# Kernel tuning notes

Hardware: AMD Instinct MI355X
Metric: run time of the kernel (lower is better)

Reference implementation:

```python
import jax, jax.numpy as jnp
import numpy as np

B, L, D, H, OUT = 4, 2048, 1024, 8, 256
DH = D // H
EPS = 1e-12


def setup_inputs() -> dict:
    key = jax.random.key(0)
    ks = jax.random.split(key, 20)
    s = lambda fan_in: 1.0 / np.sqrt(fan_in)
    def lin(k, fin, fout):
        k1, k2 = jax.random.split(k)
        w = jax.random.uniform(k1, (fin, fout), jnp.float32, -s(fin), s(fin))
        b = jax.random.uniform(k2, (fout,), jnp.float32, -s(fin), s(fin))
        return w, b
    x = jax.random.normal(ks[0], (B, L, D), jnp.float32)
    wq, bq = lin(ks[1], D, D)
    wk, bk = lin(ks[2], D, D)
    wv, bv = lin(ks[3], D, D)
    gamma = jnp.ones((D,), jnp.float32)
    beta = jnp.zeros((D,), jnp.float32)
    wff, bff = lin(ks[4], D, D)
    wc1, bc1 = lin(ks[5], D, D)
    wc2, bc2 = lin(ks[6], D, 1)
    wl1, bl1 = lin(ks[7], L, L)
    wl2, bl2 = lin(ks[8], L, OUT)
    return dict(x=x, wq=wq, bq=bq, wk=wk, bk=bk, wv=wv, bv=bv,
                gamma=gamma, beta=beta, wff=wff, bff=bff,
                wc1=wc1, bc1=bc1, wc2=wc2, bc2=bc2,
                wl1=wl1, bl1=bl1, wl2=wl2, bl2=bl2)


def layernorm(x, gamma, beta):
    mean = x.mean(-1, keepdims=True)
    var = ((x - mean) ** 2).mean(-1, keepdims=True)  # biased variance
    return gamma * (x - mean) / jnp.sqrt(var + EPS) + beta


def reference(x, wq, bq, wk, bk, wv, bv, gamma, beta, wff, bff,
              wc1, bc1, wc2, bc2, wl1, bl1, wl2, bl2):
    # multi-head self-attention (dropout = identity at inference)
    q = (x @ wq + bq).reshape(B, L, H, DH)
    k = (x @ wk + bk).reshape(B, L, H, DH)
    v = (x @ wv + bv).reshape(B, L, H, DH)
    scores = jnp.einsum('bqhd,bkhd->bhqk', q, k) / np.sqrt(DH)
    attn = jax.nn.softmax(scores, axis=-1)                  # [B,H,L,L]
    ctx = jnp.einsum('bhqk,bkhd->bqhd', attn, v).reshape(B, L, D)
    h = layernorm(x + ctx, gamma, beta)
    # feedforward: Linear + ReLU (hidden = d_model), residual + same layernorm params
    ff = jax.nn.relu(h @ wff + bff)
    h = layernorm(h + ff, gamma, beta)
    # collapse d_model -> 1
    c = jax.nn.relu(h @ wc1 + bc1)
    c = jax.nn.relu(c @ wc2 + bc2)                          # [B,L,1]
    c = jnp.squeeze(c, axis=-1)                             # [B,L]
    # collapse length -> out_featuresize
    c = jax.nn.relu(c @ wl1 + bl1)
    out = c @ wl2 + bl2                                     # [B,OUT]
    return out
```

## Files before the change

### kernel.cpp

```cpp
#include <hip/hip_runtime.h>

typedef unsigned short u16;
typedef unsigned int u32;
typedef __attribute__((ext_vector_type(4))) float f32x4;
typedef __attribute__((ext_vector_type(8))) short short8;
typedef __attribute__((ext_vector_type(4))) u32 u32x4;
typedef __attribute__((ext_vector_type(4))) u16 u16x4;

#define BB 4
#define LL 2048
#define DD 1024
#define HH 8
#define DHH 128

__device__ __forceinline__ u16 f2b(float f) {
  u32 u = __builtin_bit_cast(u32, f);
  u += 0x7fffu + ((u >> 16) & 1u);
  return (u16)(u >> 16);
}
__device__ __forceinline__ float b2f(u16 h) {
  u32 u = ((u32)h) << 16;
  return __builtin_bit_cast(float, u);
}
__device__ __forceinline__ float exp2_fast(float x) {
  float r;
  asm("v_exp_f32 %0, %1" : "=v"(r) : "v"(x));
  return r;
}
__device__ __forceinline__ u32 packbf(float a, float b) {
  return (u32)f2b(a) | ((u32)f2b(b) << 16);
}
__device__ __forceinline__ u32 bperm(int srcLane, u32 v) {
  return (u32)__builtin_amdgcn_ds_bpermute(srcLane << 2, (int)v);
}

#define GLDS16(g, l)                                                          \
  __builtin_amdgcn_global_load_lds(                                           \
      (const __attribute__((address_space(1))) void*)(g),                     \
      (__attribute__((address_space(3))) void*)(l), 16, 0, 0)

__global__ __launch_bounds__(256) void cvt_k(const float* __restrict__ X,
                                             u16* __restrict__ Xb, long n) {
  long i = ((long)blockIdx.x * 256 + threadIdx.x) * 4;
  if (i >= n) return;
  f32x4 v = *(const f32x4*)(X + i);
  u16x4 o;
#pragma unroll
  for (int k = 0; k < 4; k++) o[k] = f2b(v[k]);
  *(u16x4*)(Xb + i) = o;
}

__global__ __launch_bounds__(256) void tr_k(const float* __restrict__ W,
                                            u16* __restrict__ WT) {
  __shared__ float tile[32][33];
  const int bx = blockIdx.x, by = blockIdx.y;
  const int tx = threadIdx.x & 31, ty = threadIdx.x >> 5;
#pragma unroll
  for (int i = 0; i < 4; i++)
    tile[ty + i * 8][tx] =
        W[(long)(by * 32 + ty + i * 8) * 1024 + bx * 32 + tx];
  __syncthreads();
#pragma unroll
  for (int i = 0; i < 4; i++)
    WT[(long)(bx * 32 + ty + i * 8) * 1024 + by * 32 + tx] =
        f2b(tile[tx][ty + i * 8]);
}

template <bool RELU, int OMODE>
__global__ __launch_bounds__(256, 2) void gemm_k(
    const u16* __restrict__ A, const u16* __restrict__ BT,
    const float* __restrict__ bias, float scale, float* __restrict__ Cf,
    u16* __restrict__ Cb, int M, int N, int K) {
  __shared__ u16 As[128 * 32];
  __shared__ u16 Bs[128 * 32];
  const int nwg = gridDim.x * gridDim.y;
  const int bid = blockIdx.x + blockIdx.y * gridDim.x;
  const int swz = (bid & 7) * (nwg >> 3) + (bid >> 3);
  const int bxi = swz % gridDim.x, byi = swz / gridDim.x;
  const int t = threadIdx.x;
  const int l = t & 63, w = t >> 6;
  const int lr = l & 15, lg = l >> 4;
  const int wr = (w >> 1) * 64, wc = (w & 1) * 64;
  const long bm = (long)byi * 128, bn = (long)bxi * 128;
  const int srow = l >> 2;
  const int scol = (l & 3) * 8;
  const u16* Ag0 = A + (bm + w * 32 + srow) * (long)K + scol;
  const u16* Ag1 = A + (bm + w * 32 + 16 + srow) * (long)K + scol;
  const u16* Bg0 = BT + (bn + w * 32 + srow) * (long)K + scol;
  const u16* Bg1 = BT + (bn + w * 32 + 16 + srow) * (long)K + scol;
  u16* Al0 = As + w * 1024;
  u16* Al1 = As + w * 1024 + 512;
  u16* Bl0 = Bs + w * 1024;
  u16* Bl1 = Bs + w * 1024 + 512;
  f32x4 acc[4][4] = {};
  for (int k0 = 0; k0 < K; k0 += 32) {
    GLDS16(Ag0 + k0, Al0);
    GLDS16(Ag1 + k0, Al1);
    GLDS16(Bg0 + k0, Bl0);
    GLDS16(Bg1 + k0, Bl1);
    __syncthreads();
    short8 af[4], bf[4];
#pragma unroll
    for (int i = 0; i < 4; i++)
      af[i] = *(const short8*)&As[(wr + i * 16 + lr) * 32 + lg * 8];
#pragma unroll
    for (int i = 0; i < 4; i++)
      bf[i] = *(const short8*)&Bs[(wc + i * 16 + lr) * 32 + lg * 8];
#pragma unroll
    for (int i = 0; i < 4; i++)
#pragma unroll
      for (int j = 0; j < 4; j++)
        acc[i][j] = __builtin_amdgcn_mfma_f32_16x16x32_bf16(af[i], bf[j],
                                                            acc[i][j], 0, 0, 0);
    __syncthreads();
  }
#pragma unroll
  for (int i = 0; i < 4; i++)
#pragma unroll
    for (int j = 0; j < 4; j++) {
      long col = bn + wc + j * 16 + lr;
      float bv = bias[col];
      if (OMODE == 2) {
        long row0 = bm + wr + i * 16 + lg * 4;
        long b = row0 >> 11, l0 = row0 & 2047;
        u16x4 ov;
#pragma unroll
        for (int r = 0; r < 4; r++) {
          float v2 = (acc[i][j][r] + bv) * scale;
          if (RELU) v2 = fmaxf(v2, 0.f);
          ov[r] = f2b(v2);
        }
        *(u16x4*)(Cb + (b * 1024 + col) * 2048 + l0) = ov;
      } else {
#pragma unroll
        for (int r = 0; r < 4; r++) {
          long row = bm + wr + i * 16 + lg * 4 + r;
          float v2 = (acc[i][j][r] + bv) * scale;
          if (RELU) v2 = fmaxf(v2, 0.f);
          if (OMODE == 1)
            Cb[row * N + col] = f2b(v2);
          else
            Cf[row * N + col] = v2;
        }
      }
    }
}

__global__ __launch_bounds__(512, 4) void flash_k(const u16* __restrict__ Q,
                                                  const u16* __restrict__ Kb,
                                                  const u16* __restrict__ VT,
                                                  float* __restrict__ ctx) {
  __shared__ u16 Ks[2][64][136];
  __shared__ u16 VTs[2][128][72];
  const int nwg = gridDim.x * gridDim.y;
  const int bid = blockIdx.x + blockIdx.y * gridDim.x;
  const int swz = (bid & 7) * (nwg >> 3) + (bid >> 3);
  const int bxi = swz % gridDim.x, byi = swz / gridDim.x;
  const int t = threadIdx.x;
  const int l = t & 63, w = t >> 6;
  const int lr = l & 15, lg = l >> 4;
  const int b = byi >> 3, h = byi & 7;
  const long kbase = ((long)b * LL) * DD + h * DHH;
  const long vtbase = ((long)(b * 8 + h) * DHH) * LL;
  const int q0 = bxi * 128;

  short8 qf[4];
  {
    const u16* qp = Q + kbase + (long)(q0 + w * 16 + lr) * DD + lg * 8;
#pragma unroll
    for (int c = 0; c < 4; c++) qf[c] = *(const short8*)(qp + c * 32);
  }
  f32x4 oacc[8] = {};
  float mprev = -1e30f;
  float lsum = 0.f;

  const int krow = t >> 3, kcol = (t & 7) * 16;
  const int vrow = t >> 2, vcol = (t & 3) * 16;
  u32x4 kr0, kr1, vr0, vr1;
  {
    const u16* kp = Kb + kbase + (long)krow * DD + kcol;
    kr0 = *(const u32x4*)(kp);
    kr1 = *(const u32x4*)(kp + 8);
    const u16* vp = VT + vtbase + (long)vrow * LL + vcol;
    vr0 = *(const u32x4*)(vp);
    vr1 = *(const u32x4*)(vp + 8);
    *(u32x4*)&Ks[0][krow][kcol] = kr0;
    *(u32x4*)&Ks[0][krow][kcol + 8] = kr1;
    *(u32x4*)&VTs[0][vrow][vcol] = vr0;
    *(u32x4*)&VTs[0][vrow][vcol + 8] = vr1;
  }
  const int NT = LL / 64;
  for (int it = 0; it < NT; ++it) {
    const int cur = it & 1;
    if (it + 1 < NT) {
      const u16* kp = Kb + kbase + (long)((it + 1) * 64 + krow) * DD + kcol;
      kr0 = *(const u32x4*)(kp);
      kr1 = *(const u32x4*)(kp + 8);
      const u16* vp = VT + vtbase + (long)vrow * LL + (it + 1) * 64 + vcol;
      vr0 = *(const u32x4*)(vp);
      vr1 = *(const u32x4*)(vp + 8);
    }
    __syncthreads();

    f32x4 s[4] = {};
#pragma unroll
    for (int jc = 0; jc < 4; jc++)
#pragma unroll
      for (int c = 0; c < 4; c++) {
        short8 kf = *(const short8*)&Ks[cur][jc * 16 + lr][c * 32 + lg * 8];
        s[jc] =
            __builtin_amdgcn_mfma_f32_16x16x32_bf16(kf, qf[c], s[jc], 0, 0, 0);
      }

    float mx = fmaxf(fmaxf(s[0][0], s[0][1]), fmaxf(s[0][2], s[0][3]));
#pragma unroll
    for (int jc = 1; jc < 4; jc++)
      mx = fmaxf(mx, fmaxf(fmaxf(s[jc][0], s[jc][1]),
                           fmaxf(s[jc][2], s[jc][3])));
    mx = fmaxf(mx, __shfl_xor(mx, 16, 64));
    mx = fmaxf(mx, __shfl_xor(mx, 32, 64));

    if (__any((int)(mx > mprev + 8.f))) {
      float mn = fmaxf(mprev, mx);
      float alpha = exp2_fast(mprev - mn);
      mprev = mn;
      lsum *= alpha;
      float ar[4];
#pragma unroll
      for (int r = 0; r < 4; r++) ar[r] = __shfl(alpha, lg * 4 + r, 64);
#pragma unroll
      for (int d8 = 0; d8 < 8; d8++)
#pragma unroll
        for (int r = 0; r < 4; r++) oacc[d8][r] *= ar[r];
    }

    u32 pk2[4][2];
    float ladd = 0.f;
#pragma unroll
    for (int jc = 0; jc < 4; jc++) {
      float p0 = exp2_fast(s[jc][0] - mprev);
      float p1 = exp2_fast(s[jc][1] - mprev);
      float p2 = exp2_fast(s[jc][2] - mprev);
      float p3 = exp2_fast(s[jc][3] - mprev);
      ladd += (p0 + p1) + (p2 + p3);
      pk2[jc][0] = packbf(p0, p1);
      pk2[jc][1] = packbf(p2, p3);
    }
    lsum += ladd;

    short8 pf[2];
#pragma unroll
    for (int kk = 0; kk < 2; kk++) {
      u32x4 afv;
#pragma unroll
      for (int m = 0; m < 4; m++) {
        int srcl = lr + ((((lg & 1) << 1) + (m >> 1)) << 4);
        u32 a0 = bperm(srcl, pk2[2 * kk][m & 1]);
        u32 a1 = bperm(srcl, pk2[2 * kk + 1][m & 1]);
        afv[m] = (lg >> 1) ? a1 : a0;
      }
      pf[kk] = __builtin_bit_cast(short8, afv);
    }

#pragma unroll
    for (int kk = 0; kk < 2; kk++)
#pragma unroll
      for (int d8 = 0; d8 < 8; d8++) {
        short8 vf = *(const short8*)&VTs[cur][d8 * 16 + lr][kk * 32 + lg * 8];
        oacc[d8] =
            __builtin_amdgcn_mfma_f32_16x16x32_bf16(pf[kk], vf, oacc[d8], 0,
                                                    0, 0);
      }

    if (it + 1 < NT) {
      *(u32x4*)&Ks[cur ^ 1][krow][kcol] = kr0;
      *(u32x4*)&Ks[cur ^ 1][krow][kcol + 8] = kr1;
      *(u32x4*)&VTs[cur ^ 1][vrow][vcol] = vr0;
      *(u32x4*)&VTs[cur ^ 1][vrow][vcol + 8] = vr1;
    }
  }

  lsum += __shfl_xor(lsum, 16, 64);
  lsum += __shfl_xor(lsum, 32, 64);
#pragma unroll
  for (int r = 0; r < 4; r++) {
    float inv = 1.f / __shfl(lsum, lg * 4 + r, 64);
    float* cp = ctx + kbase + (long)(q0 + w * 16 + lg * 4 + r) * DD;
#pragma unroll
    for (int d8 = 0; d8 < 8; d8++) cp[d8 * 16 + lr] = oacc[d8][r] * inv;
  }
}

__global__ __launch_bounds__(256) void ln_k(const float* __restrict__ X,
                                            const float* __restrict__ R,
                                            const float* __restrict__ gamma,
                                            const float* __restrict__ beta,
                                            float* __restrict__ Hf,
                                            u16* __restrict__ Hb) {
  const int row = blockIdx.x, t = threadIdx.x;
  const long off = (long)row * DD + t * 4;
  f32x4 v = *(const f32x4*)(X + off);
  f32x4 rv = *(const f32x4*)(R + off);
#pragma unroll
  for (int i = 0; i < 4; i++) v[i] += rv[i];
  float s = v[0] + v[1] + v[2] + v[3];
  float q = v[0] * v[0] + v[1] * v[1] + v[2] * v[2] + v[3] * v[3];
#pragma unroll
  for (int m = 32; m >= 1; m >>= 1) {
    s += __shfl_xor(s, m, 64);
    q += __shfl_xor(q, m, 64);
  }
  __shared__ float red[8];
  if ((t & 63) == 0) {
    red[t >> 6] = s;
    red[4 + (t >> 6)] = q;
  }
  __syncthreads();
  s = red[0] + red[1] + red[2] + red[3];
  q = red[4] + red[5] + red[6] + red[7];
  const float mean = s * (1.f / 1024.f);
  const float var = q * (1.f / 1024.f) - mean * mean;
  const float rstd = rsqrtf(var + 1e-12f);
  f32x4 g = *(const f32x4*)(gamma + t * 4);
  f32x4 be = *(const f32x4*)(beta + t * 4);
  f32x4 o;
#pragma unroll
  for (int i = 0; i < 4; i++) o[i] = g[i] * (v[i] - mean) * rstd + be[i];
  if (Hf) *(f32x4*)(Hf + off) = o;
  if (Hb) {
    u16x4 ob;
#pragma unroll
    for (int i = 0; i < 4; i++) ob[i] = f2b(o[i]);
    *(u16x4*)(Hb + off) = ob;
  }
}

__global__ __launch_bounds__(256) void c2_k(const u16* __restrict__ C,
                                            const float* __restrict__ wc2,
                                            const float* __restrict__ bc2,
                                            float* __restrict__ cvec) {
  const int row = blockIdx.x, t = threadIdx.x;
  u16x4 cv = *(const u16x4*)(C + (long)row * DD + t * 4);
  f32x4 wv = *(const f32x4*)(wc2 + t * 4);
  float s = b2f(cv[0]) * wv[0] + b2f(cv[1]) * wv[1] + b2f(cv[2]) * wv[2] +
            b2f(cv[3]) * wv[3];
#pragma unroll
  for (int m = 32; m >= 1; m >>= 1) s += __shfl_xor(s, m, 64);
  __shared__ float red[4];
  if ((t & 63) == 0) red[t >> 6] = s;
  __syncthreads();
  if (t == 0)
    cvec[row] = fmaxf(red[0] + red[1] + red[2] + red[3] + bc2[0], 0.f);
}

__global__ __launch_bounds__(256) void smm_part(const float* __restrict__ Cin,
                                                const float* __restrict__ W,
                                                float* __restrict__ P, int Lr,
                                                int N, int SL) {
  const int j = blockIdx.x * 256 + threadIdx.x;
  const int l0 = blockIdx.y * SL;
  float a0 = 0, a1 = 0, a2 = 0, a3 = 0;
  for (int ll = l0; ll < l0 + SL; ll++) {
    float wv = W[(long)ll * N + j];
    a0 += Cin[ll] * wv;
    a1 += Cin[Lr + ll] * wv;
    a2 += Cin[2 * Lr + ll] * wv;
    a3 += Cin[3 * Lr + ll] * wv;
  }
  float* Pp = P + ((long)blockIdx.y * 4) * N + j;
  Pp[0] = a0;
  Pp[N] = a1;
  Pp[2 * N] = a2;
  Pp[3 * N] = a3;
}

template <bool RELU>
__global__ __launch_bounds__(256) void smm_red(const float* __restrict__ P,
                                               const float* __restrict__ bias,
                                               float* __restrict__ Out, int N,
                                               int S) {
  const int j = blockIdx.x * 256 + threadIdx.x;
#pragma unroll
  for (int b = 0; b < 4; b++) {
    float a = 0;
    for (int s = 0; s < S; s++) a += P[((long)s * 4 + b) * N + j];
    a += bias[j];
    if (RELU) a = fmaxf(a, 0.f);
    Out[(long)b * N + j] = a;
  }
}

extern "C" void kernel_launch(void* const* d_in, const int* in_sizes, int n_in,
                              void* d_out, int out_size, void* d_ws,
                              size_t ws_size, hipStream_t stream) {
  (void)in_sizes; (void)n_in; (void)out_size; (void)ws_size;
  const float* x = (const float*)d_in[0];
  const float* wq = (const float*)d_in[1];
  const float* bq = (const float*)d_in[2];
  const float* wk = (const float*)d_in[3];
  const float* bk = (const float*)d_in[4];
  const float* wv = (const float*)d_in[5];
  const float* bv = (const float*)d_in[6];
  const float* gamma = (const float*)d_in[7];
  const float* beta = (const float*)d_in[8];
  const float* wff = (const float*)d_in[9];
  const float* bff = (const float*)d_in[10];
  const float* wc1 = (const float*)d_in[11];
  const float* bc1 = (const float*)d_in[12];
  const float* wc2 = (const float*)d_in[13];
  const float* bc2 = (const float*)d_in[14];
  const float* wl1 = (const float*)d_in[15];
  const float* bl1 = (const float*)d_in[16];
  const float* wl2 = (const float*)d_in[17];
  const float* bl2 = (const float*)d_in[18];

  char* wsp = (char*)d_ws;
  size_t off = 0;
  auto take = [&](size_t bytes) -> char* {
    char* p = wsp + off;
    off += (bytes + 255) & ~(size_t)255;
    return p;
  };
  u16* xb = (u16*)take((size_t)8192 * 1024 * 2);
  u16* wqT = (u16*)take((size_t)1024 * 1024 * 2);
  u16* wkT = (u16*)take((size_t)1024 * 1024 * 2);
  u16* wvT = (u16*)take((size_t)1024 * 1024 * 2);
  u16* wffT = (u16*)take((size_t)1024 * 1024 * 2);
  u16* wc1T = (u16*)take((size_t)1024 * 1024 * 2);
  u16* qb = (u16*)take((size_t)8192 * 1024 * 2);
  u16* kbuf = (u16*)take((size_t)8192 * 1024 * 2);
  u16* vT = (u16*)take((size_t)8192 * 1024 * 2);
  float* ctxb = (float*)take((size_t)8192 * 1024 * 4);
  float* h1f = (float*)take((size_t)8192 * 1024 * 4);
  float* cvec = (float*)take(8192 * 4);
  float* c3 = (float*)take(8192 * 4);
  float* P1 = (float*)take((size_t)16 * 4 * 2048 * 4);
  float* P2 = (float*)take((size_t)16 * 4 * 256 * 4);
  u16* h1b = qb;
  u16* h2b = kbuf;
  u16* cb = vT;
  float* ff = ctxb;

  cvt_k<<<8192, 256, 0, stream>>>(x, xb, (long)8192 * 1024);
  dim3 trg(32, 32);
  tr_k<<<trg, 256, 0, stream>>>(wq, wqT);
  tr_k<<<trg, 256, 0, stream>>>(wk, wkT);
  tr_k<<<trg, 256, 0, stream>>>(wv, wvT);
  tr_k<<<trg, 256, 0, stream>>>(wff, wffT);
  tr_k<<<trg, 256, 0, stream>>>(wc1, wc1T);

  dim3 gg(8, 64);
  gemm_k<false, 1><<<gg, 256, 0, stream>>>(
      xb, wqT, bq, 0.12751743f, nullptr, qb, 8192, 1024, 1024);
  gemm_k<false, 1><<<gg, 256, 0, stream>>>(xb, wkT, bk, 1.f, nullptr, kbuf,
                                           8192, 1024, 1024);
  gemm_k<false, 2><<<gg, 256, 0, stream>>>(xb, wvT, bv, 1.f, nullptr, vT,
                                           8192, 1024, 1024);
  flash_k<<<dim3(16, 32), 512, 0, stream>>>(qb, kbuf, vT, ctxb);
  ln_k<<<8192, 256, 0, stream>>>(x, ctxb, gamma, beta, h1f, h1b);
  gemm_k<true, 0><<<gg, 256, 0, stream>>>(h1b, wffT, bff, 1.f, ff, nullptr,
                                          8192, 1024, 1024);
  ln_k<<<8192, 256, 0, stream>>>(h1f, ff, gamma, beta, nullptr, h2b);
  gemm_k<true, 1><<<gg, 256, 0, stream>>>(h2b, wc1T, bc1, 1.f, nullptr, cb,
                                          8192, 1024, 1024);
  c2_k<<<8192, 256, 0, stream>>>(cb, wc2, bc2, cvec);
  smm_part<<<dim3(8, 16), 256, 0, stream>>>(cvec, wl1, P1, 2048, 2048, 128);
  smm_red<true><<<8, 256, 0, stream>>>(P1, bl1, c3, 2048, 16);
  smm_part<<<dim3(1, 16), 256, 0, stream>>>(c3, wl2, P2, 2048, 256, 128);
  smm_red<false><<<1, 256, 0, stream>>>(P2, bl2, (float*)d_out, 256, 16);
}
```

Baseline: 399.6 us.

## Double-buffer LDS tiles in bf16 GEMM to overlap global loads with MFMA

The GEMM kernel now keeps two LDS buffers for the A and B tiles. It issues the global-to-LDS loads for the next K-step before computing on the current one, and drops one barrier per iteration. The aim is to hide global memory latency behind the MFMA work. The cost is double the LDS use (32KB per block), which may reduce occupancy. Correctness also depends on the GLDS loads completing before the single barrier at the end of each iteration.

```diff
diff --git a/kernel.cpp b/kernel.cpp
--- a/kernel.cpp
+++ b/kernel.cpp
@@ -71,8 +71,8 @@
     const u16* __restrict__ A, const u16* __restrict__ BT,
     const float* __restrict__ bias, float scale, float* __restrict__ Cf,
     u16* __restrict__ Cb, int M, int N, int K) {
-  __shared__ u16 As[128 * 32];
-  __shared__ u16 Bs[128 * 32];
+  __shared__ u16 As[2][128 * 32];
+  __shared__ u16 Bs[2][128 * 32];
   const int nwg = gridDim.x * gridDim.y;
   const int bid = blockIdx.x + blockIdx.y * gridDim.x;
   const int swz = (bid & 7) * (nwg >> 3) + (bid >> 3);
@@ -88,24 +88,29 @@
   const u16* Ag1 = A + (bm + w * 32 + 16 + srow) * (long)K + scol;
   const u16* Bg0 = BT + (bn + w * 32 + srow) * (long)K + scol;
   const u16* Bg1 = BT + (bn + w * 32 + 16 + srow) * (long)K + scol;
-  u16* Al0 = As + w * 1024;
-  u16* Al1 = As + w * 1024 + 512;
-  u16* Bl0 = Bs + w * 1024;
-  u16* Bl1 = Bs + w * 1024 + 512;
+  const int wo = w * 1024;
   f32x4 acc[4][4] = {};
+  GLDS16(Ag0, &As[0][wo]);
+  GLDS16(Ag1, &As[0][wo + 512]);
+  GLDS16(Bg0, &Bs[0][wo]);
+  GLDS16(Bg1, &Bs[0][wo + 512]);
+  __syncthreads();
+  int cur = 0;
   for (int k0 = 0; k0 < K; k0 += 32) {
-    GLDS16(Ag0 + k0, Al0);
-    GLDS16(Ag1 + k0, Al1);
-    GLDS16(Bg0 + k0, Bl0);
-    GLDS16(Bg1 + k0, Bl1);
-    __syncthreads();
+    const int nxt = cur ^ 1;
+    if (k0 + 32 < K) {
+      GLDS16(Ag0 + k0 + 32, &As[nxt][wo]);
+      GLDS16(Ag1 + k0 + 32, &As[nxt][wo + 512]);
+      GLDS16(Bg0 + k0 + 32, &Bs[nxt][wo]);
+      GLDS16(Bg1 + k0 + 32, &Bs[nxt][wo + 512]);
+    }
     short8 af[4], bf[4];
 #pragma unroll
     for (int i = 0; i < 4; i++)
-      af[i] = *(const short8*)&As[(wr + i * 16 + lr) * 32 + lg * 8];
+      af[i] = *(const short8*)&As[cur][(wr + i * 16 + lr) * 32 + lg * 8];
 #pragma unroll
     for (int i = 0; i < 4; i++)
-      bf[i] = *(const short8*)&Bs[(wc + i * 16 + lr) * 32 + lg * 8];
+      bf[i] = *(const short8*)&Bs[cur][(wc + i * 16 + lr) * 32 + lg * 8];
 #pragma unroll
     for (int i = 0; i < 4; i++)
 #pragma unroll
@@ -113,6 +118,7 @@
         acc[i][j] = __builtin_amdgcn_mfma_f32_16x16x32_bf16(af[i], bf[j],
                                                             acc[i][j], 0, 0, 0);
     __syncthreads();
+    cur = nxt;
   }
 #pragma unroll
   for (int i = 0; i < 4; i++)
```

Result: no change. 402.1 us (+0.6%).
